# Kernel tuning notes

Measured on AMD Instinct MI355X. Metric: run time of the kernel, lower is better.

## Reference

```python
import jax, jax.numpy as jnp
import numpy as np

N_NODES = 50000
IN_DIM = 128
OUT_DIM = 128
HEADS = 4
HEAD_DIM = OUT_DIM // HEADS
N_EDGES = 800000
LN_EPS = 1e-5
NEG_SLOPE = 0.2


def setup_inputs() -> dict:
    key = jax.random.key(0)
    ks = jax.random.split(key, 8)
    x = jax.random.normal(ks[0], (N_NODES, IN_DIM), dtype=jnp.float32)
    edge_index = jax.random.randint(ks[1], (2, N_EDGES), 0, N_NODES, dtype=jnp.int64)
    s = 1.0 / np.sqrt(IN_DIM)
    W = jax.random.uniform(ks[2], (IN_DIM, HEADS * HEAD_DIM), jnp.float32, -s, s)
    att_src = jax.random.uniform(ks[3], (HEADS, HEAD_DIM), jnp.float32, -s, s)
    att_dst = jax.random.uniform(ks[4], (HEADS, HEAD_DIM), jnp.float32, -s, s)
    bias = jnp.zeros((OUT_DIM,), jnp.float32)
    gamma = jnp.ones((OUT_DIM,), jnp.float32)
    beta = jnp.zeros((OUT_DIM,), jnp.float32)
    return {"x": x, "edge_index": edge_index, "W": W, "att_src": att_src,
            "att_dst": att_dst, "bias": bias, "gamma": gamma, "beta": beta}


def reference(x, edge_index, W, att_src, att_dst, bias, gamma, beta):
    N = x.shape[0]
    H, C = att_src.shape
    # add self-loops (PyG GATConv default)
    loops = jnp.arange(N, dtype=edge_index.dtype)
    src = jnp.concatenate([edge_index[0], loops])  # [E+N]
    dst = jnp.concatenate([edge_index[1], loops])

    h = (x @ W).reshape(N, H, C)                      # [N,H,C]
    a_src = jnp.einsum('nhc,hc->nh', h, att_src)      # [N,H]
    a_dst = jnp.einsum('nhc,hc->nh', h, att_dst)

    e = jax.nn.leaky_relu(a_src[src] + a_dst[dst], NEG_SLOPE)   # [E+N,H]
    emax = jax.ops.segment_max(e, dst, num_segments=N)          # [N,H]
    ex = jnp.exp(e - emax[dst])
    denom = jax.ops.segment_sum(ex, dst, num_segments=N)
    alpha = ex / denom[dst]                                     # [E+N,H]

    msg = h[src] * alpha[:, :, None]                            # [E+N,H,C]
    out = jax.ops.segment_sum(msg, dst, num_segments=N).reshape(N, H * C) + bias

    # LayerNorm
    mu = out.mean(-1, keepdims=True)
    var = ((out - mu) ** 2).mean(-1, keepdims=True)
    hn = (out - mu) / jnp.sqrt(var + LN_EPS) * gamma + beta

    # residual is Identity (in_dim == out_dim); GELU exact; dropout = eval identity
    return jax.nn.gelu(hn + x, approximate=False)
```

## Files before the change

### kernel.cpp

```cpp
#include <hip/hip_runtime.h>
#include <math.h>

#define N_NODES 50000
#define HEADS 4
#define NEG_SLOPE 0.2f
#define LN_EPS 1e-5f
#define SLOTS 80
#define GR 32
#define EPB 2048


__device__ __forceinline__ void load_edge(const int* __restrict__ ei, int e, int E,
                                          int is64, int& s, int& d) {
    if (is64) {
        s = ei[2 * e];
        d = ei[2 * (E + e)];
    } else {
        s = ei[e];
        d = ei[E + e];
    }
}

__device__ __forceinline__ int detect_is64(const int* __restrict__ ei, int t, int* s_flag) {
    if (t < 64) {
        int nz = (ei[2 * t + 1] != 0) ? 1 : 0;
        unsigned long long b = __ballot(nz);
        if (t == 0) *s_flag = (b == 0ULL) ? 1 : 0;
    }
    __syncthreads();
    return *s_flag;
}

__device__ __forceinline__ float s8f(unsigned u, int p) {
    return (float)((int)(u << (24 - 8 * p)) >> 24);
}

__device__ __forceinline__ float edge_w(float v) {
    v = v > 0.f ? v : NEG_SLOPE * v;
    return __expf(v);
}

__device__ __forceinline__ void scatter_one(const int* __restrict__ ei, int e, int E,
                                            int is64, int* __restrict__ cnt,
                                            unsigned short* __restrict__ esrc) {
    if (e >= E) return;
    int s, d;
    load_edge(ei, e, E, is64, s, d);
    int p = atomicAdd(&cnt[d], 1);
    if (p < SLOTS) __builtin_nontemporal_store((unsigned short)s, &esrc[d * SLOTS + p]);
}


__global__ __launch_bounds__(256) void gemm_scatter_kernel(
    const float* __restrict__ x, const float* __restrict__ W,
    const float* __restrict__ att_src, const float* __restrict__ att_dst,
    unsigned* __restrict__ hb, float* __restrict__ hscale,
    float* __restrict__ a_src, float* __restrict__ a_dst,
    const int* __restrict__ ei, int E, int nScatter, int nGemm,
    int* __restrict__ cnt, unsigned short* __restrict__ esrc) {
    __shared__ float sX[GR * 128];
    const int t = threadIdx.x;
    const int b = (int)blockIdx.x;

    const bool isScatter = (b % 5) == 0;
    const int rid = isScatter ? (b / 5) : (4 * (b / 5) + (b % 5) - 1);

    if (isScatter) {
        if (rid >= nScatter) return;
        int is64 = detect_is64(ei, t, (int*)sX);
        const int e0 = rid * EPB + t;
#pragma unroll
        for (int u = 0; u < 8; ++u)
            scatter_one(ei, e0 + u * 256, E, is64, cnt, esrc);
        return;
    }

    if (rid >= nGemm) return;
    const int rowBase = rid * GR;
    const int nRows = min(GR, N_NODES - rowBase);

    const float4* x4 = (const float4*)(x + (size_t)rowBase * 128);
    float4* sX4 = (float4*)sX;
    for (int i = t; i < nRows * 32; i += 256) sX4[i] = x4[i];
    __syncthreads();

    const int tx = t & 31;
    const int ty = t >> 5;
    float acc[4][4];
#pragma unroll
    for (int r = 0; r < 4; ++r) { acc[r][0] = acc[r][1] = acc[r][2] = acc[r][3] = 0.f; }

    const float4* W4 = (const float4*)W;
    for (int k = 0; k < 128; k += 4) {
        float4 w0 = W4[(k + 0) * 32 + tx];
        float4 w1 = W4[(k + 1) * 32 + tx];
        float4 w2 = W4[(k + 2) * 32 + tx];
        float4 w3 = W4[(k + 3) * 32 + tx];
#pragma unroll
        for (int r = 0; r < 4; ++r) {
            const float* xr = &sX[(ty * 4 + r) * 128 + k];
            float a0 = xr[0], a1 = xr[1], a2 = xr[2], a3 = xr[3];
            acc[r][0] += a0 * w0.x + a1 * w1.x + a2 * w2.x + a3 * w3.x;
            acc[r][1] += a0 * w0.y + a1 * w1.y + a2 * w2.y + a3 * w3.y;
            acc[r][2] += a0 * w0.z + a1 * w1.z + a2 * w2.z + a3 * w3.z;
            acc[r][3] += a0 * w0.w + a1 * w1.w + a2 * w2.w + a3 * w3.w;
        }
    }

    const float4 as4 = ((const float4*)att_src)[tx];
    const float4 ad4 = ((const float4*)att_dst)[tx];
    const int hd = tx >> 3;
#pragma unroll
    for (int r = 0; r < 4; ++r) {
        int row = rowBase + ty * 4 + r;
        float4 av = make_float4(acc[r][0], acc[r][1], acc[r][2], acc[r][3]);

        float m = fmaxf(fmaxf(fabsf(av.x), fabsf(av.y)),
                        fmaxf(fabsf(av.z), fabsf(av.w)));
#pragma unroll
        for (int o = 1; o < 32; o <<= 1) m = fmaxf(m, __shfl_xor(m, o, 64));
        m = fmaxf(m, 1e-20f);
        const float sc = m * (1.0f / 127.0f);
        const float inv = 127.0f / m;

        if (row < N_NODES) {
            int q0 = __float2int_rn(av.x * inv);
            int q1 = __float2int_rn(av.y * inv);
            int q2 = __float2int_rn(av.z * inv);
            int q3 = __float2int_rn(av.w * inv);
            unsigned pk = (unsigned)(q0 & 255) | ((unsigned)(q1 & 255) << 8) |
                          ((unsigned)(q2 & 255) << 16) | ((unsigned)q3 << 24);
            hb[(size_t)row * 32 + tx] = pk;
            if (tx == 0) hscale[row] = sc;
        }

        float sp = av.x * as4.x + av.y * as4.y + av.z * as4.z + av.w * as4.w;
        float dp = av.x * ad4.x + av.y * ad4.y + av.z * ad4.z + av.w * ad4.w;
#pragma unroll
        for (int o = 1; o < 8; o <<= 1) {
            sp += __shfl_xor(sp, o, 64);
            dp += __shfl_xor(dp, o, 64);
        }
        if ((tx & 7) == 0 && row < N_NODES) {
            a_src[row * 4 + hd] = sp;
            a_dst[row * 4 + hd] = dp;
        }
    }
}

__global__ __launch_bounds__(256) void gat_fused_kernel(
    const int* __restrict__ cnt, const unsigned short* __restrict__ esrc,
    const float* __restrict__ a_src, const float* __restrict__ a_dst,
    const unsigned* __restrict__ hb, const float* __restrict__ hscale,
    const float* __restrict__ bias, const float* __restrict__ x,
    const float* __restrict__ gamma, const float* __restrict__ beta,
    float* __restrict__ out) {
    const int t = threadIdx.x;
    const int l = t & 63;
    const int wv = t >> 6;
    const int g = l >> 4;
    const int j = l & 15;
    const int n = blockIdx.x * 16 + wv * 4 + g;
    const int hh = j >> 2;

    const uint2* hb2 = (const uint2*)hb;

    const float adst_me = a_dst[(n << 2) + hh];
    float ps = edge_w(a_src[(n << 2) + hh] + adst_me);

    uint2 hvS = hb2[(unsigned)(n * 16 + j)];
    {
        const float uS = ps * hscale[n];
        float acc0 = uS * s8f(hvS.x, 0), acc1 = uS * s8f(hvS.x, 1);
        float acc2 = uS * s8f(hvS.x, 2), acc3 = uS * s8f(hvS.x, 3);
        float acc4 = uS * s8f(hvS.y, 0), acc5 = uS * s8f(hvS.y, 1);
        float acc6 = uS * s8f(hvS.y, 2), acc7 = uS * s8f(hvS.y, 3);

        const int deg = min(cnt[n], SLOTS);
        const unsigned short* row = esrc + n * SLOTS;

        for (int base = 0; base < deg; base += 8) {
            const int rem = deg - base;
            uint4 q = *(const uint4*)(row + base);
            int s0 = (int)(q.x & 0xffffu);
            int s1 = (rem > 1) ? (int)(q.x >> 16) : n;
            int s2 = (rem > 2) ? (int)(q.y & 0xffffu) : n;
            int s3 = (rem > 3) ? (int)(q.y >> 16) : n;
            int s4 = (rem > 4) ? (int)(q.z & 0xffffu) : n;
            int s5 = (rem > 5) ? (int)(q.z >> 16) : n;
            int s6 = (rem > 6) ? (int)(q.w & 0xffffu) : n;
            int s7 = (rem > 7) ? (int)(q.w >> 16) : n;

            float b0 = a_src[(s0 << 2) + hh];
            float b1 = a_src[(s1 << 2) + hh];
            float b2 = a_src[(s2 << 2) + hh];
            float b3 = a_src[(s3 << 2) + hh];
            float b4 = a_src[(s4 << 2) + hh];
            float b5 = a_src[(s5 << 2) + hh];
            float b6 = a_src[(s6 << 2) + hh];
            float b7 = a_src[(s7 << 2) + hh];
            float c0 = hscale[s0], c1 = hscale[s1], c2 = hscale[s2], c3 = hscale[s3];
            float c4 = hscale[s4], c5 = hscale[s5], c6 = hscale[s6], c7 = hscale[s7];
            uint2 h0 = hb2[(unsigned)(s0 * 16 + j)];
            uint2 h1 = hb2[(unsigned)(s1 * 16 + j)];
            uint2 h2 = hb2[(unsigned)(s2 * 16 + j)];
            uint2 h3 = hb2[(unsigned)(s3 * 16 + j)];
            uint2 h4 = hb2[(unsigned)(s4 * 16 + j)];
            uint2 h5 = hb2[(unsigned)(s5 * 16 + j)];
            uint2 h6 = hb2[(unsigned)(s6 * 16 + j)];
            uint2 h7 = hb2[(unsigned)(s7 * 16 + j)];

            float w0 = edge_w(b0 + adst_me);
            float w1 = (rem > 1) ? edge_w(b1 + adst_me) : 0.f;
            float w2 = (rem > 2) ? edge_w(b2 + adst_me) : 0.f;
            float w3 = (rem > 3) ? edge_w(b3 + adst_me) : 0.f;
            float w4 = (rem > 4) ? edge_w(b4 + adst_me) : 0.f;
            float w5 = (rem > 5) ? edge_w(b5 + adst_me) : 0.f;
            float w6 = (rem > 6) ? edge_w(b6 + adst_me) : 0.f;
            float w7 = (rem > 7) ? edge_w(b7 + adst_me) : 0.f;
            ps += (w0 + w1 + w2 + w3) + (w4 + w5 + w6 + w7);

            float u0 = w0 * c0, u1 = w1 * c1, u2 = w2 * c2, u3 = w3 * c3;
            float u4 = w4 * c4, u5 = w5 * c5, u6 = w6 * c6, u7 = w7 * c7;

            acc0 += u0 * s8f(h0.x, 0) + u1 * s8f(h1.x, 0) + u2 * s8f(h2.x, 0) + u3 * s8f(h3.x, 0)
                  + u4 * s8f(h4.x, 0) + u5 * s8f(h5.x, 0) + u6 * s8f(h6.x, 0) + u7 * s8f(h7.x, 0);
            acc1 += u0 * s8f(h0.x, 1) + u1 * s8f(h1.x, 1) + u2 * s8f(h2.x, 1) + u3 * s8f(h3.x, 1)
                  + u4 * s8f(h4.x, 1) + u5 * s8f(h5.x, 1) + u6 * s8f(h6.x, 1) + u7 * s8f(h7.x, 1);
            acc2 += u0 * s8f(h0.x, 2) + u1 * s8f(h1.x, 2) + u2 * s8f(h2.x, 2) + u3 * s8f(h3.x, 2)
                  + u4 * s8f(h4.x, 2) + u5 * s8f(h5.x, 2) + u6 * s8f(h6.x, 2) + u7 * s8f(h7.x, 2);
            acc3 += u0 * s8f(h0.x, 3) + u1 * s8f(h1.x, 3) + u2 * s8f(h2.x, 3) + u3 * s8f(h3.x, 3)
                  + u4 * s8f(h4.x, 3) + u5 * s8f(h5.x, 3) + u6 * s8f(h6.x, 3) + u7 * s8f(h7.x, 3);
            acc4 += u0 * s8f(h0.y, 0) + u1 * s8f(h1.y, 0) + u2 * s8f(h2.y, 0) + u3 * s8f(h3.y, 0)
                  + u4 * s8f(h4.y, 0) + u5 * s8f(h5.y, 0) + u6 * s8f(h6.y, 0) + u7 * s8f(h7.y, 0);
            acc5 += u0 * s8f(h0.y, 1) + u1 * s8f(h1.y, 1) + u2 * s8f(h2.y, 1) + u3 * s8f(h3.y, 1)
                  + u4 * s8f(h4.y, 1) + u5 * s8f(h5.y, 1) + u6 * s8f(h6.y, 1) + u7 * s8f(h7.y, 1);
            acc6 += u0 * s8f(h0.y, 2) + u1 * s8f(h1.y, 2) + u2 * s8f(h2.y, 2) + u3 * s8f(h3.y, 2)
                  + u4 * s8f(h4.y, 2) + u5 * s8f(h5.y, 2) + u6 * s8f(h6.y, 2) + u7 * s8f(h7.y, 2);
            acc7 += u0 * s8f(h0.y, 3) + u1 * s8f(h1.y, 3) + u2 * s8f(h2.y, 3) + u3 * s8f(h3.y, 3)
                  + u4 * s8f(h4.y, 3) + u5 * s8f(h5.y, 3) + u6 * s8f(h6.y, 3) + u7 * s8f(h7.y, 3);
        }

        const float inv = 1.0f / ps;
        const float4* bias4 = (const float4*)bias;
        float4 bA = bias4[j * 2], bB = bias4[j * 2 + 1];
        float v0 = acc0 * inv + bA.x, v1 = acc1 * inv + bA.y;
        float v2 = acc2 * inv + bA.z, v3 = acc3 * inv + bA.w;
        float v4 = acc4 * inv + bB.x, v5 = acc5 * inv + bB.y;
        float v6 = acc6 * inv + bB.z, v7 = acc7 * inv + bB.w;

        float s1 = v0 + v1 + v2 + v3 + v4 + v5 + v6 + v7;
        float s2 = v0 * v0 + v1 * v1 + v2 * v2 + v3 * v3 +
                   v4 * v4 + v5 * v5 + v6 * v6 + v7 * v7;
#pragma unroll
        for (int o = 1; o < 16; o <<= 1) {
            s1 += __shfl_xor(s1, o, 64);
            s2 += __shfl_xor(s2, o, 64);
        }
        float mu = s1 * (1.0f / 128.0f);
        float var = s2 * (1.0f / 128.0f) - mu * mu;
        float rstd = rsqrtf(var + LN_EPS);

        const float4* gamma4 = (const float4*)gamma;
        const float4* beta4 = (const float4*)beta;
        const float4* x4 = (const float4*)x;
        float4 gA = gamma4[j * 2], gB = gamma4[j * 2 + 1];
        float4 eA = beta4[j * 2], eB = beta4[j * 2 + 1];
        float4 xA = x4[(size_t)n * 32 + j * 2], xB = x4[(size_t)n * 32 + j * 2 + 1];

        float r0 = (v0 - mu) * rstd * gA.x + eA.x + xA.x;
        float r1 = (v1 - mu) * rstd * gA.y + eA.y + xA.y;
        float r2 = (v2 - mu) * rstd * gA.z + eA.z + xA.z;
        float r3 = (v3 - mu) * rstd * gA.w + eA.w + xA.w;
        float r4 = (v4 - mu) * rstd * gB.x + eB.x + xB.x;
        float r5 = (v5 - mu) * rstd * gB.y + eB.y + xB.y;
        float r6 = (v6 - mu) * rstd * gB.z + eB.z + xB.z;
        float r7 = (v7 - mu) * rstd * gB.w + eB.w + xB.w;

        const float k = 0.70710678118654752440f;
        float4 oA = make_float4(0.5f * r0 * (1.0f + erff(r0 * k)),
                                0.5f * r1 * (1.0f + erff(r1 * k)),
                                0.5f * r2 * (1.0f + erff(r2 * k)),
                                0.5f * r3 * (1.0f + erff(r3 * k)));
        float4 oB = make_float4(0.5f * r4 * (1.0f + erff(r4 * k)),
                                0.5f * r5 * (1.0f + erff(r5 * k)),
                                0.5f * r6 * (1.0f + erff(r6 * k)),
                                0.5f * r7 * (1.0f + erff(r7 * k)));
        float4* out4 = (float4*)out;
        out4[(size_t)n * 32 + j * 2] = oA;
        out4[(size_t)n * 32 + j * 2 + 1] = oB;
    }
}


extern "C" void kernel_launch(void* const* d_in, const int* in_sizes, int n_in,
                              void* d_out, int out_size, void* d_ws, size_t ws_size,
                              hipStream_t stream) {
    const float* x       = (const float*)d_in[0];
    const int*   ei      = (const int*)d_in[1];
    const float* W       = (const float*)d_in[2];
    const float* att_src = (const float*)d_in[3];
    const float* att_dst = (const float*)d_in[4];
    const float* bias    = (const float*)d_in[5];
    const float* gamma   = (const float*)d_in[6];
    const float* beta    = (const float*)d_in[7];
    float* out = (float*)d_out;
    const int E = in_sizes[1] / 2;

    unsigned* hb         = (unsigned*)d_ws;
    float* hscale        = (float*)(hb + (size_t)N_NODES * 32);
    float* a_src         = hscale + N_NODES;
    float* a_dst         = a_src + N_NODES * 4;
    int*   cnt           = (int*)(a_dst + N_NODES * 4);
    unsigned short* esrc = (unsigned short*)(cnt + N_NODES);

    const int nScatter = (E + EPB - 1) / EPB;
    const int nGemm = (N_NODES + GR - 1) / GR;
    int total = 5 * nScatter;
    const int needGemm = 5 * ((nGemm + 3) / 4);
    if (needGemm > total) total = needGemm;

    hipMemsetAsync(cnt, 0, N_NODES * sizeof(int), stream);
    gemm_scatter_kernel<<<total, 256, 0, stream>>>(
        x, W, att_src, att_dst, hb, hscale, a_src, a_dst, ei, E, nScatter, nGemm,
        cnt, esrc);
    gat_fused_kernel<<<N_NODES / 16, 256, 0, stream>>>(cnt, esrc, a_src, a_dst, hb,
                                                       hscale, bias, x, gamma, beta, out);
}
```

Baseline: 176.7 us.

## Compute node projection with bf16 MFMA and restage int8 output through LDS

Replaces the FP32 FMA GEMM for x@W with bf16 MFMA 16x16x32 instructions. W is converted to bf16 into a swizzled LDS layout per block, and x rows are loaded straight from global and converted in registers. Rows per GEMM block go from 32 to 64, and the scatter/GEMM block interleave changes from 1:4 to 1:2. The int8-quantized output is staged through LDS so it can be written coalesced. Each block reconverts W, and bf16 inputs lower the precision of h and the attention logits.

```diff
diff --git a/kernel.cpp b/kernel.cpp
--- a/kernel.cpp
+++ b/kernel.cpp
@@ -6,9 +6,17 @@
 #define NEG_SLOPE 0.2f
 #define LN_EPS 1e-5f
 #define SLOTS 80
-#define GR 32
+#define GR 64
 #define EPB 2048
 
+typedef short short8 __attribute__((ext_vector_type(8)));
+typedef float f32x4 __attribute__((ext_vector_type(4)));
+
+
+__device__ __forceinline__ short f2bf(float f) {
+    unsigned u = __float_as_uint(f);
+    return (short)((u + 0x7fffu + ((u >> 16) & 1u)) >> 16);
+}
 
 __device__ __forceinline__ void load_edge(const int* __restrict__ ei, int e, int E,
                                           int is64, int& s, int& d) {
@@ -47,27 +55,27 @@
     int s, d;
     load_edge(ei, e, E, is64, s, d);
     int p = atomicAdd(&cnt[d], 1);
-    if (p < SLOTS) __builtin_nontemporal_store((unsigned short)s, &esrc[d * SLOTS + p]);
-}
-
-
-__global__ __launch_bounds__(256) void gemm_scatter_kernel(
+    if (p < SLOTS) esrc[d * SLOTS + p] = (unsigned short)s;
+}
+
+
+__global__ __launch_bounds__(256, 4) void gemm_scatter_kernel(
     const float* __restrict__ x, const float* __restrict__ W,
     const float* __restrict__ att_src, const float* __restrict__ att_dst,
     unsigned* __restrict__ hb, float* __restrict__ hscale,
     float* __restrict__ a_src, float* __restrict__ a_dst,
     const int* __restrict__ ei, int E, int nScatter, int nGemm,
     int* __restrict__ cnt, unsigned short* __restrict__ esrc) {
-    __shared__ float sX[GR * 128];
+    __shared__ __align__(16) char smem[40960];
     const int t = threadIdx.x;
     const int b = (int)blockIdx.x;
 
-    const bool isScatter = (b % 5) == 0;
-    const int rid = isScatter ? (b / 5) : (4 * (b / 5) + (b % 5) - 1);
+    const bool isScatter = (b % 3) == 0;
+    const int rid = isScatter ? (b / 3) : (2 * (b / 3) + (b % 3) - 1);
 
     if (isScatter) {
         if (rid >= nScatter) return;
-        int is64 = detect_is64(ei, t, (int*)sX);
+        int is64 = detect_is64(ei, t, (int*)smem);
         const int e0 = rid * EPB + t;
 #pragma unroll
         for (int u = 0; u < 8; ++u)
@@ -77,74 +85,114 @@
 
     if (rid >= nGemm) return;
     const int rowBase = rid * GR;
-    const int nRows = min(GR, N_NODES - rowBase);
-
-    const float4* x4 = (const float4*)(x + (size_t)rowBase * 128);
-    float4* sX4 = (float4*)sX;
-    for (int i = t; i < nRows * 32; i += 256) sX4[i] = x4[i];
+    const int l = t & 63;
+    const int wv = t >> 6;
+
+    {
+        const int nlo = l & 7, khi = l >> 3;
+        for (int i = 0; i < 8; ++i) {
+            int tile = wv + 4 * i;
+            int n = (tile & 15) * 8 + nlo;
+            int k8 = (tile >> 4) * 8 + khi;
+            short8 pk;
+#pragma unroll
+            for (int jj = 0; jj < 8; ++jj)
+                pk[jj] = f2bf(W[(k8 * 8 + jj) * 128 + n]);
+            int us = (k8 & 8) | ((k8 & 7) ^ (n & 7));
+            *(short8*)(smem + n * 256 + us * 16) = pk;
+        }
+    }
     __syncthreads();
 
-    const int tx = t & 31;
-    const int ty = t >> 5;
-    float acc[4][4];
-#pragma unroll
-    for (int r = 0; r < 4; ++r) { acc[r][0] = acc[r][1] = acc[r][2] = acc[r][3] = 0.f; }
-
-    const float4* W4 = (const float4*)W;
-    for (int k = 0; k < 128; k += 4) {
-        float4 w0 = W4[(k + 0) * 32 + tx];
-        float4 w1 = W4[(k + 1) * 32 + tx];
-        float4 w2 = W4[(k + 2) * 32 + tx];
-        float4 w3 = W4[(k + 3) * 32 + tx];
-#pragma unroll
-        for (int r = 0; r < 4; ++r) {
-            const float* xr = &sX[(ty * 4 + r) * 128 + k];
-            float a0 = xr[0], a1 = xr[1], a2 = xr[2], a3 = xr[3];
-            acc[r][0] += a0 * w0.x + a1 * w1.x + a2 * w2.x + a3 * w3.x;
-            acc[r][1] += a0 * w0.y + a1 * w1.y + a2 * w2.y + a3 * w3.y;
-            acc[r][2] += a0 * w0.z + a1 * w1.z + a2 * w2.z + a3 * w3.z;
-            acc[r][3] += a0 * w0.w + a1 * w1.w + a2 * w2.w + a3 * w3.w;
-        }
-    }
-
-    const float4 as4 = ((const float4*)att_src)[tx];
-    const float4 ad4 = ((const float4*)att_dst)[tx];
-    const int hd = tx >> 3;
+    const int g = l >> 4;
+    const int c = l & 15;
+
+    f32x4 acc[8];
+#pragma unroll
+    for (int ct = 0; ct < 8; ++ct) acc[ct] = {0.f, 0.f, 0.f, 0.f};
+
+    {
+        int arow = rowBase + wv * 16 + c;
+        if (arow >= N_NODES) arow = N_NODES - 1;
+        const float* xrow = x + (size_t)arow * 128;
+#pragma unroll
+        for (int kk = 0; kk < 4; ++kk) {
+            float4 xa = *(const float4*)(xrow + kk * 32 + g * 8);
+            float4 xb = *(const float4*)(xrow + kk * 32 + g * 8 + 4);
+            short8 af;
+            af[0] = f2bf(xa.x); af[1] = f2bf(xa.y); af[2] = f2bf(xa.z); af[3] = f2bf(xa.w);
+            af[4] = f2bf(xb.x); af[5] = f2bf(xb.y); af[6] = f2bf(xb.z); af[7] = f2bf(xb.w);
+#pragma unroll
+            for (int ct = 0; ct < 8; ++ct) {
+                int n = ct * 16 + c;
+                int u = kk * 4 + g;
+                int us = (u & 8) | ((u & 7) ^ (n & 7));
+                short8 bf = *(const short8*)(smem + n * 256 + us * 16);
+                acc[ct] = __builtin_amdgcn_mfma_f32_16x16x32_bf16(af, bf, acc[ct], 0, 0, 0);
+            }
+        }
+    }
+
+    char* ep = smem + 32768 + wv * 2048;
+    float asA[4], asB[4], adA[4], adB[4];
+#pragma unroll
+    for (int h = 0; h < 4; ++h) {
+        asA[h] = att_src[h * 32 + c];
+        asB[h] = att_src[h * 32 + 16 + c];
+        adA[h] = att_dst[h * 32 + c];
+        adB[h] = att_dst[h * 32 + 16 + c];
+    }
 #pragma unroll
     for (int r = 0; r < 4; ++r) {
-        int row = rowBase + ty * 4 + r;
-        float4 av = make_float4(acc[r][0], acc[r][1], acc[r][2], acc[r][3]);
-
-        float m = fmaxf(fmaxf(fabsf(av.x), fabsf(av.y)),
-                        fmaxf(fabsf(av.z), fabsf(av.w)));
-#pragma unroll
-        for (int o = 1; o < 32; o <<= 1) m = fmaxf(m, __shfl_xor(m, o, 64));
+        float v[8];
+#pragma unroll
+        for (int ct = 0; ct < 8; ++ct) v[ct] = acc[ct][r];
+
+        float m = fabsf(v[0]);
+#pragma unroll
+        for (int ct = 1; ct < 8; ++ct) m = fmaxf(m, fabsf(v[ct]));
+#pragma unroll
+        for (int o = 1; o < 16; o <<= 1) m = fmaxf(m, __shfl_xor(m, o, 64));
         m = fmaxf(m, 1e-20f);
-        const float sc = m * (1.0f / 127.0f);
         const float inv = 127.0f / m;
 
-        if (row < N_NODES) {
-            int q0 = __float2int_rn(av.x * inv);
-            int q1 = __float2int_rn(av.y * inv);
-            int q2 = __float2int_rn(av.z * inv);
-            int q3 = __float2int_rn(av.w * inv);
-            unsigned pk = (unsigned)(q0 & 255) | ((unsigned)(q1 & 255) << 8) |
-                          ((unsigned)(q2 & 255) << 16) | ((unsigned)q3 << 24);
-            hb[(size_t)row * 32 + tx] = pk;
-            if (tx == 0) hscale[row] = sc;
-        }
-
-        float sp = av.x * as4.x + av.y * as4.y + av.z * as4.z + av.w * as4.w;
-        float dp = av.x * ad4.x + av.y * ad4.y + av.z * ad4.z + av.w * ad4.w;
-#pragma unroll
-        for (int o = 1; o < 8; o <<= 1) {
-            sp += __shfl_xor(sp, o, 64);
-            dp += __shfl_xor(dp, o, 64);
-        }
-        if ((tx & 7) == 0 && row < N_NODES) {
-            a_src[row * 4 + hd] = sp;
-            a_dst[row * 4 + hd] = dp;
-        }
+        float sp[4], dp[4];
+#pragma unroll
+        for (int h = 0; h < 4; ++h) {
+            sp[h] = v[2 * h] * asA[h] + v[2 * h + 1] * asB[h];
+            dp[h] = v[2 * h] * adA[h] + v[2 * h + 1] * adB[h];
+        }
+#pragma unroll
+        for (int o = 1; o < 16; o <<= 1) {
+#pragma unroll
+            for (int h = 0; h < 4; ++h) {
+                sp[h] += __shfl_xor(sp[h], o, 64);
+                dp[h] += __shfl_xor(dp[h], o, 64);
+            }
+        }
+        const int row_l = g * 4 + r;
+        const int row = rowBase + wv * 16 + row_l;
+        if (c == 0 && row < N_NODES) {
+            hscale[row] = m * (1.0f / 127.0f);
+            a_src[row * 4 + 0] = sp[0]; a_src[row * 4 + 1] = sp[1];
+            a_src[row * 4 + 2] = sp[2]; a_src[row * 4 + 3] = sp[3];
+            a_dst[row * 4 + 0] = dp[0]; a_dst[row * 4 + 1] = dp[1];
+            a_dst[row * 4 + 2] = dp[2]; a_dst[row * 4 + 3] = dp[3];
+        }
+#pragma unroll
+        for (int ct = 0; ct < 8; ++ct) {
+            int q = __float2int_rn(v[ct] * inv);
+            ep[row_l * 128 + ct * 16 + c] = (char)q;
+        }
+    }
+
+#pragma unroll
+    for (int w8 = 0; w8 < 8; ++w8) {
+        int idx = w8 * 64 + l;
+        int row_l = idx >> 5, tx = idx & 31;
+        unsigned word = *(const unsigned*)(ep + row_l * 128 + tx * 4);
+        int row = rowBase + wv * 16 + row_l;
+        if (row < N_NODES) hb[(size_t)row * 32 + tx] = word;
     }
 }
 
@@ -316,8 +364,8 @@
 
     const int nScatter = (E + EPB - 1) / EPB;
     const int nGemm = (N_NODES + GR - 1) / GR;
-    int total = 5 * nScatter;
-    const int needGemm = 5 * ((nGemm + 3) / 4);
+    int total = 3 * nScatter;
+    const int needGemm = 3 * ((nGemm + 1) / 2);
     if (needGemm > total) total = needGemm;
 
     hipMemsetAsync(cnt, 0, N_NODES * sizeof(int), stream);
```

New measurement: 167.0 us. 5.5% less time.
